# Performance work log

Measured on AMD Instinct MI355X. Metric: run time of the kernel, lower is better.

## Reference

```python
import jax, jax.numpy as jnp
import numpy as np
from jax import lax

N, L, D, F = 16, 512, 256, 256
KW = 3
EPS = 1e-5


def setup_inputs() -> dict:
    key = jax.random.key(0)
    ks = jax.random.split(key, 12)
    return {
        "x": jax.random.normal(ks[0], (N, L, D), jnp.float32),
        "conv1_w": jax.random.normal(ks[1], (F, D, KW), jnp.float32) * 0.05,
        "conv1_b": jnp.zeros((F,), jnp.float32),
        "ln1_g": jnp.ones((F,), jnp.float32),
        "ln1_b": jnp.zeros((F,), jnp.float32),
        "conv2_w": jax.random.normal(ks[2], (F, F, KW), jnp.float32) * 0.05,
        "conv2_b": jnp.zeros((F,), jnp.float32),
        "ln2_g": jnp.ones((F,), jnp.float32),
        "ln2_b": jnp.zeros((F,), jnp.float32),
        "lin_w": jax.random.normal(ks[3], (F, 1), jnp.float32) * 0.05,
        "lin_b": jnp.zeros((1,), jnp.float32),
        "target": jax.random.randint(ks[4], (N, L), 1, 8, jnp.int32),
        "mel_max_length": 4096,
    }


def _layernorm(h, g, b):
    m = jnp.mean(h, axis=-1, keepdims=True)
    v = jnp.var(h, axis=-1, keepdims=True)
    return (h - m) * lax.rsqrt(v + EPS) * g + b


def _conv1d(h, w, b):
    # h: [N, L, C_in]; w: [C_out, C_in, K]; 'same' padding=1 for K=3
    y = lax.conv_general_dilated(h.transpose(0, 2, 1), w, (1,), [(1, 1)],
                                 dimension_numbers=("NCH", "OIH", "NCH"))
    return (y + b[None, :, None]).transpose(0, 2, 1)


def _duration_predictor(x, c1w, c1b, g1, b1, c2w, c2b, g2, b2, lw, lb):
    h = jax.nn.relu(_layernorm(_conv1d(x, c1w, c1b), g1, b1))
    h = jax.nn.relu(_layernorm(_conv1d(h, c2w, c2b), g2, b2))
    return jax.nn.relu(h @ lw + lb)[..., 0]  # [N, L]


def _length_regulate(x, dur, T):
    # Equivalent to one-hot alignment @ x, done as a duration-indexed gather.
    cum = jnp.cumsum(dur, axis=-1)                       # [N, L]
    t = jnp.arange(T, dtype=cum.dtype)                   # [T]
    idx = jax.vmap(lambda c: jnp.searchsorted(c, t, side="right"))(cum)  # [N, T]
    valid = t[None, :] < cum[:, -1:]                     # [N, T]
    out = jnp.take_along_axis(x, jnp.clip(idx, 0, x.shape[1] - 1)[:, :, None], axis=1)
    return jnp.where(valid[..., None], out, jnp.zeros((), x.dtype))


def reference(x, conv1_w, conv1_b, ln1_g, ln1_b, conv2_w, conv2_b, ln2_g, ln2_b,
              lin_w, lin_b, target, mel_max_length):
    dpo = _duration_predictor(x, conv1_w, conv1_b, ln1_g, ln1_b,
                              conv2_w, conv2_b, ln2_g, ln2_b, lin_w, lin_b)
    out = _length_regulate(x, target, mel_max_length)    # [N, mel_max_length, D]
    return (out, dpo)
```

## Files before the change

kernel.cpp:

```cpp
#include <hip/hip_runtime.h>
#include <hip/hip_bf16.h>

using u16 = unsigned short;
typedef __bf16 bf16x8 __attribute__((ext_vector_type(8)));
typedef float f32x4 __attribute__((ext_vector_type(4)));

#define N_B   16
#define L_S   512
#define D_F   256
#define T_MEL 4096
#define M_TOT (N_B * L_S)
#define OUT_ELEMS ((size_t)N_B * T_MEL * D_F)
#define H1_ELEMS  ((size_t)M_TOT * D_F)
#define WP_ELEMS  (24 * 8192)
#define TBLK 128

__device__ __forceinline__ u16 f2bf(float f) {
  __hip_bfloat16 h = __float2bfloat16(f);
  return *(u16*)&h;
}

__device__ __forceinline__ bf16x8 pack8(float4 v0, float4 v1) {
  union { bf16x8 h; u16 u[8]; } r;
  r.u[0] = f2bf(v0.x); r.u[1] = f2bf(v0.y); r.u[2] = f2bf(v0.z); r.u[3] = f2bf(v0.w);
  r.u[4] = f2bf(v1.x); r.u[5] = f2bf(v1.y); r.u[6] = f2bf(v1.z); r.u[7] = f2bf(v1.w);
  return r.h;
}

__global__ __launch_bounds__(256)
void pack_kernel(const float* __restrict__ w1, const float* __restrict__ w2,
                 u16* __restrict__ wp1, u16* __restrict__ wp2) {
  int o   = (int)blockIdx.x * 256 + (int)threadIdx.x;
  int s   = o >> 13;
  int rem = o & 8191;
  int f   = rem >> 5;
  int ki  = rem & 31;
  int d   = ((s & 7) << 5) + ki;
  int tap = s >> 3;
  int src = f * 768 + d * 3 + tap;
  wp1[o] = f2bf(w1[src]);
  wp2[o] = f2bf(w2[src]);
}

template<int STAGE>
__device__ __forceinline__ void conv_body(
    const int blk, const int t,
    const float* __restrict__ Xf, const u16* __restrict__ Xh,
    const u16* __restrict__ Wp,
    const float* __restrict__ cb,  const float* __restrict__ lgm,
    const float* __restrict__ lbt, const float* __restrict__ lw,
    const float* __restrict__ lb,  u16* __restrict__ Hout,
    float* __restrict__ dpo,
    u16* As, u16* Bs, float* sBias, float* sG, float* sB, float* sLw,
    float (*redS)[4][16], float (*redQ)[4][16])
{
  if (t < 256) {
    sBias[t] = cb[t];
    sG[t]    = lgm[t];
    sB[t]    = lbt[t];
    if (STAGE == 2) sLw[t] = lw[t];
  }

  const int m0   = blk * 32;
  const int n    = m0 >> 9;
  const int l0   = m0 & 511;
  const int wave = t >> 6, lane = t & 63;
  const int cs   = wave & 3;
  const int rh   = wave >> 2;
  const int wc   = cs * 64;
  const int rh16 = rh * 16;
  const int p    = lane & 15, q = lane >> 4;

  for (int c = t; c < 1088; c += 512) {
    int row  = c >> 5;
    int col8 = c & 31;
    int l    = l0 + row - 1;
    uint4 val;
    if ((unsigned)l < 512u) {
      if (STAGE == 1) {
        const float* src = Xf + (((size_t)((n << 9) + l)) << 8) + (col8 << 3);
        float4 v0 = *(const float4*)src;
        float4 v1 = *(const float4*)(src + 4);
        bf16x8 pk = pack8(v0, v1);
        __builtin_memcpy(&val, &pk, 16);
      } else {
        val = *(const uint4*)(Xh + (((size_t)((n << 9) + l)) << 8) + (col8 << 3));
      }
    } else {
      val = make_uint4(0u, 0u, 0u, 0u);
    }
    *(uint4*)(As + row * 264 + (col8 << 3)) = val;
  }
  {
    uint4 r0 = *(const uint4*)(Wp + (t << 3));
    uint4 r1 = *(const uint4*)(Wp + ((t + 512) << 3));
    *(uint4*)(Bs + (t << 3))         = r0;
    *(uint4*)(Bs + ((t + 512) << 3)) = r1;
  }
  __syncthreads();

  f32x4 acc[4];
  #pragma unroll
  for (int i = 0; i < 4; i++) acc[i] = (f32x4){0.f, 0.f, 0.f, 0.f};

  for (int s = 0; s < 24; s++) {
    const int cur = s & 1;
    uint4 r0, r1;
    if (s < 23) {
      const u16* src = Wp + ((size_t)(s + 1) << 13);
      r0 = *(const uint4*)(src + (t << 3));
      r1 = *(const uint4*)(src + ((t + 512) << 3));
    }
    {
      const u16* bs = Bs + (cur << 13);
      const int tap = s >> 3, dbase = (s & 7) << 5;
      bf16x8 af = *(const bf16x8*)(As + (rh16 + p + tap) * 264 + dbase + (q << 3));
      #pragma unroll
      for (int ct = 0; ct < 4; ct++) {
        bf16x8 bfr = *(const bf16x8*)(bs + ((wc + ct * 16 + p) << 5) + (q << 3));
        acc[ct] = __builtin_amdgcn_mfma_f32_16x16x32_bf16(af, bfr, acc[ct], 0, 0, 0);
      }
    }
    if (s < 23) {
      __syncthreads();
      *(uint4*)(Bs + ((cur ^ 1) << 13) + (t << 3))         = r0;
      *(uint4*)(Bs + ((cur ^ 1) << 13) + ((t + 512) << 3)) = r1;
      __syncthreads();
    }
  }

  float s0[4] = {0,0,0,0}, s1[4] = {0,0,0,0};
  #pragma unroll
  for (int ct = 0; ct < 4; ct++) {
    float bias = sBias[wc + ct * 16 + p];
    #pragma unroll
    for (int j = 0; j < 4; j++) {
      float v = acc[ct][j] + bias;
      acc[ct][j] = v;
      s0[j] += v;
      s1[j] += v * v;
    }
  }
  #pragma unroll
  for (int m = 1; m <= 8; m <<= 1) {
    #pragma unroll
    for (int j = 0; j < 4; j++) {
      s0[j] += __shfl_xor(s0[j], m);
      s1[j] += __shfl_xor(s1[j], m);
    }
  }
  if (p == 0) {
    #pragma unroll
    for (int j = 0; j < 4; j++) {
      redS[rh][cs][q * 4 + j] = s0[j];
      redQ[rh][cs][q * 4 + j] = s1[j];
    }
  }
  __syncthreads();
  float mean[4], rstd[4];
  #pragma unroll
  for (int j = 0; j < 4; j++) {
    int r = q * 4 + j;
    float S = redS[rh][0][r] + redS[rh][1][r] + redS[rh][2][r] + redS[rh][3][r];
    float Q = redQ[rh][0][r] + redQ[rh][1][r] + redQ[rh][2][r] + redQ[rh][3][r];
    float mu  = S * (1.0f / 256.0f);
    float var = Q * (1.0f / 256.0f) - mu * mu;
    mean[j] = mu;
    rstd[j] = rsqrtf(var + 1e-5f);
  }

  if (STAGE == 1) {
    #pragma unroll
    for (int ct = 0; ct < 4; ct++) {
      int c = wc + ct * 16 + p;
      float gg = sG[c], bb = sB[c];
      #pragma unroll
      for (int j = 0; j < 4; j++) {
        float v = (acc[ct][j] - mean[j]) * rstd[j] * gg + bb;
        v = fmaxf(v, 0.0f);
        Hout[(size_t)(m0 + rh16 + q * 4 + j) * 256 + c] = f2bf(v);
      }
    }
  } else {
    float ls[4] = {0,0,0,0};
    #pragma unroll
    for (int ct = 0; ct < 4; ct++) {
      int c = wc + ct * 16 + p;
      float gg = sG[c], bb = sB[c], ww = sLw[c];
      #pragma unroll
      for (int j = 0; j < 4; j++) {
        float v = (acc[ct][j] - mean[j]) * rstd[j] * gg + bb;
        v = fmaxf(v, 0.0f);
        ls[j] += v * ww;
      }
    }
    #pragma unroll
    for (int m = 1; m <= 8; m <<= 1) {
      #pragma unroll
      for (int j = 0; j < 4; j++) ls[j] += __shfl_xor(ls[j], m);
    }
    __syncthreads();
    if (p == 0) {
      #pragma unroll
      for (int j = 0; j < 4; j++) redS[rh][cs][q * 4 + j] = ls[j];
    }
    __syncthreads();
    if (t < 32) {
      int r2 = t >> 4, ri = t & 15;
      float dv = fmaxf(redS[r2][0][ri] + redS[r2][1][ri] +
                       redS[r2][2][ri] + redS[r2][3][ri] + lb[0], 0.0f);
      dpo[m0 + t] = dv;
    }
  }
}

__device__ __forceinline__ void lr_body512(
    const int lrblk, const int t,
    const float* __restrict__ X, const int* __restrict__ tgt,
    float* __restrict__ out, int* sc, int* sidx)
{
  const int n  = lrblk >> 4;
  const int t0 = (lrblk & 15) * 256;

  sc[t] = tgt[n * L_S + t];
  __syncthreads();
  for (int off = 1; off < L_S; off <<= 1) {
    int v = (t >= off) ? sc[t - off] : 0;
    __syncthreads();
    sc[t] += v;
    __syncthreads();
  }
  const int total = sc[L_S - 1];
  if (t < 256) {
    int tt = t0 + t;
    int lo = 0, hi = L_S;
    while (lo < hi) {
      int mid = (lo + hi) >> 1;
      if (sc[mid] <= tt) lo = mid + 1; else hi = mid;
    }
    sidx[t] = (tt < total) ? lo : -1;
  }
  __syncthreads();

  #pragma unroll
  for (int i = 0; i < 32; i++) {
    int u   = t + i * 512;
    int dg  = u & 63;
    int tr  = u >> 6;
    int idx = sidx[tr];
    float4 v = make_float4(0.f, 0.f, 0.f, 0.f);
    if (idx >= 0)
      v = *(const float4*)(X + (((size_t)(n * L_S + idx)) << 8) + dg * 4);
    *(float4*)(out + (((size_t)(n * T_MEL + t0 + tr)) << 8) + dg * 4) = v;
  }
}

template<int STAGE>
__global__ __launch_bounds__(512)
void conv_ln_kernel(const float* __restrict__ Xf, const u16* __restrict__ Xh,
                    const u16* __restrict__ Wp,
                    const float* __restrict__ cb,  const float* __restrict__ lgm,
                    const float* __restrict__ lbt, const float* __restrict__ lw,
                    const float* __restrict__ lb,  u16* __restrict__ Hout,
                    float* __restrict__ dpo)
{
  __shared__ __align__(16) u16 As[34 * 264 + 8];
  __shared__ __align__(16) u16 Bs[2 * 8192];
  __shared__ float sBias[256], sG[256], sB[256], sLw[256];
  __shared__ float redS[2][4][16], redQ[2][4][16];
  conv_body<STAGE>((int)blockIdx.x, (int)threadIdx.x, Xf, Xh, Wp, cb, lgm, lbt,
                   lw, lb, Hout, dpo, As, Bs, sBias, sG, sB, sLw, redS, redQ);
}

__global__ __launch_bounds__(512)
void conv1_lr_kernel(const float* __restrict__ x, const u16* __restrict__ Wp,
                     const float* __restrict__ cb,  const float* __restrict__ lgm,
                     const float* __restrict__ lbt, u16* __restrict__ Hout,
                     const int* __restrict__ tgt, float* __restrict__ out)
{
  __shared__ __align__(16) u16 As[34 * 264 + 8];
  __shared__ __align__(16) u16 Bs[2 * 8192];
  __shared__ float sBias[256], sG[256], sB[256], sLw[256];
  __shared__ float redS[2][4][16], redQ[2][4][16];
  __shared__ int  sc[512];
  __shared__ int  sidx[256];

  const int blk = (int)blockIdx.x, t = (int)threadIdx.x;
  if (blk < 256) {
    conv_body<1>(blk, t, x, nullptr, Wp, cb, lgm, lbt, nullptr, nullptr,
                 Hout, nullptr, As, Bs, sBias, sG, sB, sLw, redS, redQ);
  } else {
    lr_body512(blk - 256, t, x, tgt, out, sc, sidx);
  }
}

__global__ __launch_bounds__(256)
void lr_kernel(const float* __restrict__ X, const int* __restrict__ tgt,
               float* __restrict__ out) {
  __shared__ int c[L_S];
  __shared__ int sidx[TBLK];
  const int t  = threadIdx.x;
  const int n  = blockIdx.x >> 5;
  const int t0 = (blockIdx.x & 31) * TBLK;

  c[t]       = tgt[n * L_S + t];
  c[t + 256] = tgt[n * L_S + t + 256];
  __syncthreads();
  for (int off = 1; off < L_S; off <<= 1) {
    int v0 = (t >= off) ? c[t - off] : 0;
    int i1 = t + 256;
    int v1 = (i1 >= off) ? c[i1 - off] : 0;
    __syncthreads();
    c[t]  += v0;
    c[i1] += v1;
    __syncthreads();
  }
  const int total = c[L_S - 1];
  if (t < TBLK) {
    int tt = t0 + t;
    int lo = 0, hi = L_S;
    while (lo < hi) {
      int mid = (lo + hi) >> 1;
      if (c[mid] <= tt) lo = mid + 1; else hi = mid;
    }
    sidx[t] = (tt < total) ? lo : -1;
  }
  __syncthreads();

  #pragma unroll
  for (int i = 0; i < 32; i++) {
    int u   = t + i * 256;
    int dg  = u & 63;
    int tr  = u >> 6;
    int idx = sidx[tr];
    float4 v = make_float4(0.f, 0.f, 0.f, 0.f);
    if (idx >= 0)
      v = *(const float4*)(X + (((size_t)(n * L_S + idx)) << 8) + dg * 4);
    *(float4*)(out + (((size_t)(n * T_MEL + t0 + tr)) << 8) + dg * 4) = v;
  }
}

extern "C" void kernel_launch(void* const* d_in, const int* in_sizes, int n_in,
                              void* d_out, int out_size, void* d_ws, size_t ws_size,
                              hipStream_t stream) {
  (void)in_sizes; (void)n_in; (void)out_size;

  const float* x   = (const float*)d_in[0];
  const float* w1  = (const float*)d_in[1];
  const float* b1  = (const float*)d_in[2];
  const float* g1  = (const float*)d_in[3];
  const float* be1 = (const float*)d_in[4];
  const float* w2  = (const float*)d_in[5];
  const float* b2  = (const float*)d_in[6];
  const float* g2  = (const float*)d_in[7];
  const float* be2 = (const float*)d_in[8];
  const float* lw  = (const float*)d_in[9];
  const float* lb  = (const float*)d_in[10];
  const int*   tgt = (const int*)d_in[11];

  float* out = (float*)d_out;
  float* dpo = out + OUT_ELEMS;

  const size_t need = (H1_ELEMS + 2 * (size_t)WP_ELEMS) * sizeof(u16);

  if (d_ws != nullptr && ws_size >= need) {
    u16* h1  = (u16*)d_ws;
    u16* wp1 = h1 + H1_ELEMS;
    u16* wp2 = wp1 + WP_ELEMS;
    pack_kernel<<<768, 256, 0, stream>>>(w1, w2, wp1, wp2);
    conv1_lr_kernel<<<512, 512, 0, stream>>>(x, wp1, b1, g1, be1, h1, tgt, out);
    conv_ln_kernel<2><<<M_TOT / 32, 512, 0, stream>>>(
        nullptr, h1, wp2, b2, g2, be2, lw, lb, nullptr, dpo);
  } else {
    u16* h1  = (u16*)d_out;
    u16* wp1 = h1 + H1_ELEMS;
    u16* wp2 = wp1 + WP_ELEMS;
    pack_kernel<<<768, 256, 0, stream>>>(w1, w2, wp1, wp2);
    conv_ln_kernel<1><<<M_TOT / 32, 512, 0, stream>>>(
        x, nullptr, wp1, b1, g1, be1, nullptr, nullptr, h1, nullptr);
    conv_ln_kernel<2><<<M_TOT / 32, 512, 0, stream>>>(
        nullptr, h1, wp2, b2, g2, be2, lw, lb, nullptr, dpo);
    lr_kernel<<<N_B * (T_MEL / TBLK), 256, 0, stream>>>(x, tgt, out);
  }
}
```

Measured before the change: 128.5 us.

## Double-register prefetch of conv weight slabs with one barrier per step

The conv GEMM weight pipeline is restructured. Two weight slabs are now prefetched ahead into registers, and the loop is unrolled by two over a pair of ping-pong LDS buffers. Each K-step now needs one __syncthreads instead of two. The first two weight loads are issued before the activation tile is staged, which hides global latency behind that staging. The cost is extra register pressure from holding two slabs in flight.

```diff
diff --git a/kernel.cpp b/kernel.cpp
--- a/kernel.cpp
+++ b/kernel.cpp
@@ -71,6 +71,34 @@
   const int rh16 = rh * 16;
   const int p    = lane & 15, q = lane >> 4;
 
+  f32x4 acc[4];
+  #pragma unroll
+  for (int i = 0; i < 4; i++) acc[i] = (f32x4){0.f, 0.f, 0.f, 0.f};
+
+  auto LDW = [&](int s, uint4 &r0, uint4 &r1) {
+    const u16* src = Wp + ((size_t)s << 13);
+    r0 = *(const uint4*)(src + (t << 3));
+    r1 = *(const uint4*)(src + ((t + 512) << 3));
+  };
+  auto WRB = [&](int buf, const uint4 &r0, const uint4 &r1) {
+    *(uint4*)(Bs + (buf << 13) + (t << 3))         = r0;
+    *(uint4*)(Bs + (buf << 13) + ((t + 512) << 3)) = r1;
+  };
+  auto MF = [&](int buf, int s) {
+    const u16* bs = Bs + (buf << 13);
+    const int tap = s >> 3, dbase = (s & 7) << 5;
+    bf16x8 af = *(const bf16x8*)(As + (rh16 + p + tap) * 264 + dbase + (q << 3));
+    #pragma unroll
+    for (int ct = 0; ct < 4; ct++) {
+      bf16x8 bfr = *(const bf16x8*)(bs + ((wc + ct * 16 + p) << 5) + (q << 3));
+      acc[ct] = __builtin_amdgcn_mfma_f32_16x16x32_bf16(af, bfr, acc[ct], 0, 0, 0);
+    }
+  };
+
+  uint4 e0, e1, o0, o1;
+  LDW(0, e0, e1);
+  LDW(1, o0, o1);
+
   for (int c = t; c < 1088; c += 512) {
     int row  = c >> 5;
     int col8 = c & 31;
@@ -91,42 +119,18 @@
     }
     *(uint4*)(As + row * 264 + (col8 << 3)) = val;
   }
-  {
-    uint4 r0 = *(const uint4*)(Wp + (t << 3));
-    uint4 r1 = *(const uint4*)(Wp + ((t + 512) << 3));
-    *(uint4*)(Bs + (t << 3))         = r0;
-    *(uint4*)(Bs + ((t + 512) << 3)) = r1;
-  }
-  __syncthreads();
-
-  f32x4 acc[4];
-  #pragma unroll
-  for (int i = 0; i < 4; i++) acc[i] = (f32x4){0.f, 0.f, 0.f, 0.f};
-
-  for (int s = 0; s < 24; s++) {
-    const int cur = s & 1;
-    uint4 r0, r1;
-    if (s < 23) {
-      const u16* src = Wp + ((size_t)(s + 1) << 13);
-      r0 = *(const uint4*)(src + (t << 3));
-      r1 = *(const uint4*)(src + ((t + 512) << 3));
-    }
-    {
-      const u16* bs = Bs + (cur << 13);
-      const int tap = s >> 3, dbase = (s & 7) << 5;
-      bf16x8 af = *(const bf16x8*)(As + (rh16 + p + tap) * 264 + dbase + (q << 3));
-      #pragma unroll
-      for (int ct = 0; ct < 4; ct++) {
-        bf16x8 bfr = *(const bf16x8*)(bs + ((wc + ct * 16 + p) << 5) + (q << 3));
-        acc[ct] = __builtin_amdgcn_mfma_f32_16x16x32_bf16(af, bfr, acc[ct], 0, 0, 0);
-      }
-    }
-    if (s < 23) {
-      __syncthreads();
-      *(uint4*)(Bs + ((cur ^ 1) << 13) + (t << 3))         = r0;
-      *(uint4*)(Bs + ((cur ^ 1) << 13) + ((t + 512) << 3)) = r1;
-      __syncthreads();
-    }
+  WRB(0, e0, e1);
+  __syncthreads();
+
+  for (int s2 = 0; s2 < 24; s2 += 2) {
+    MF(0, s2);
+    if (s2 + 2 < 24) LDW(s2 + 2, e0, e1);
+    WRB(1, o0, o1);
+    __syncthreads();
+    MF(1, s2 + 1);
+    if (s2 + 3 < 24) LDW(s2 + 3, o0, o1);
+    if (s2 + 2 < 24) WRB(0, e0, e1);
+    __syncthreads();
   }
 
   float s0[4] = {0,0,0,0}, s1[4] = {0,0,0,0};
```

After: 121.0 us (median of 2 runs). 1.06x faster.
